# Performance work log

Hardware: AMD Instinct MI355X
Metric: run time of the kernel (lower is better)

The kernel has to match this reference:

```python
import jax, jax.numpy as jnp
import numpy as np

B, N, D, H, R = 4, 2048, 256, 8, 64
DH = D // H          # head dim = 32
K_SPARSE = 32        # top-k neighbors kept per query row
BN_EPS = 1e-5


def setup_inputs() -> dict:
    key = jax.random.key(0)
    ks = jax.random.split(key, 16)
    s_in = 1.0 / np.sqrt(D)
    s_r = 1.0 / np.sqrt(R)
    def lr(k1, k2):
        return (jax.random.normal(k1, (D, R), jnp.float32) * s_in,
                jax.random.normal(k2, (R, D), jnp.float32) * s_r)
    U_np, V_np = lr(ks[0], ks[1])
    U_q, V_q = lr(ks[2], ks[3])
    U_k, V_k = lr(ks[4], ks[5])
    U_v, V_v = lr(ks[6], ks[7])
    U_o, V_o = lr(ks[8], ks[9])
    U_op, V_op = lr(ks[10], ks[11])
    return {
        'x': jax.random.normal(ks[12], (B, N, D), jnp.float32),
        'U_np': U_np, 'V_np': V_np, 'b_np': jnp.zeros((D,), jnp.float32),
        'U_q': U_q, 'V_q': V_q,
        'U_k': U_k, 'V_k': V_k,
        'U_v': U_v, 'V_v': V_v,
        'U_o': U_o, 'V_o': V_o, 'b_o': jnp.zeros((D,), jnp.float32),
        'U_op': U_op, 'V_op': V_op, 'b_op': jnp.zeros((D,), jnp.float32),
        'gamma': jnp.ones((D,), jnp.float32),
        'beta': jnp.zeros((D,), jnp.float32),
    }


def _low_rank(x, U, V, b=None):
    y = (x @ U) @ V  # [..., D] -> [..., R] -> [..., D]
    return y + b if b is not None else y


def _heads(t):  # [B,N,D] -> [B,H,N,DH]
    return t.reshape(B, N, H, DH).transpose(0, 2, 1, 3)


def reference(x, U_np, V_np, b_np, U_q, V_q, U_k, V_k, U_v, V_v,
              U_o, V_o, b_o, U_op, V_op, b_op, gamma, beta):
    # node_proj: low-rank projection
    h = _low_rank(x, U_np, V_np, b_np)                      # [B,N,D]
    # low-rank sparse attention (q=k=v=h)
    q = _heads(_low_rank(h, U_q, V_q))                      # [B,H,N,DH]
    k = _heads(_low_rank(h, U_k, V_k))
    v = _heads(_low_rank(h, U_v, V_v))
    scores = jnp.einsum('bhnd,bhmd->bhnm', q, k) / jnp.sqrt(jnp.float32(DH))
    # topk sparsity: keep the K_SPARSE largest scores per query row
    thr = jax.lax.top_k(scores, K_SPARSE)[0][..., -1:]      # [B,H,N,1]
    neg_inf = jnp.finfo(scores.dtype).min
    scores = jnp.where(scores >= thr, scores, neg_inf)
    attn = jax.nn.softmax(scores, axis=-1)                  # [B,H,N,N]
    o = jnp.einsum('bhnm,bhmd->bhnd', attn, v)              # [B,H,N,DH]
    o = o.transpose(0, 2, 1, 3).reshape(B, N, D)
    o = _low_rank(o, U_o, V_o, b_o)                         # attention out proj
    # out_proj
    out = _low_rank(o, U_op, V_op, b_op)                    # [B,N,D]
    # BatchNorm1d over channel dim (stats over B and N, training-mode batch stats)
    mu = out.mean(axis=(0, 1))
    var = out.var(axis=(0, 1))
    out = (out - mu) * jax.lax.rsqrt(var + BN_EPS) * gamma + beta
    return out
```

## Files before the change

kernel.cpp:

```cpp
#include <hip/hip_runtime.h>
#include <hip/hip_bf16.h>

#define BB 4
#define NN 2048
#define DD 256
#define HH 8
#define RR 64
#define DHH 32
#define KSP 32
#define ROWS (BB*NN)
#define NEG_INF (-3.0e38f)

typedef __attribute__((ext_vector_type(8))) short bf16x8;
typedef __attribute__((ext_vector_type(4))) float f32x4;
#define MFMA16(A,B,C) __builtin_amdgcn_mfma_f32_16x16x32_bf16((A),(B),(C),0,0,0)

__global__ __launch_bounds__(64) void k_node_proj(
    const float* __restrict__ x, const float* __restrict__ U,
    const float* __restrict__ V, const float* __restrict__ bias,
    float* __restrict__ h)
{
    const int row = blockIdx.x, lane = threadIdx.x;
    __shared__ float xs[DD];
    __shared__ float ts[RR];
    const float* xr = x + (size_t)row * DD;
    { float4 t4 = ((const float4*)xr)[lane];
      xs[lane*4]=t4.x; xs[lane*4+1]=t4.y; xs[lane*4+2]=t4.z; xs[lane*4+3]=t4.w; }
    __syncthreads();
    float t = 0.f;
    for (int d = 0; d < DD; ++d) t = fmaf(xs[d], U[d*RR + lane], t);
    ts[lane] = t;
    __syncthreads();
    float a[4];
    #pragma unroll
    for (int j = 0; j < 4; ++j) a[j] = bias[lane + 64*j];
    for (int r = 0; r < RR; ++r) {
        float tv = ts[r];
        const float* Vr = V + r*DD + lane;
        #pragma unroll
        for (int j = 0; j < 4; ++j) a[j] = fmaf(tv, Vr[64*j], a[j]);
    }
    float* hr = h + (size_t)row * DD;
    #pragma unroll
    for (int j = 0; j < 4; ++j) hr[lane + 64*j] = a[j];
}

__global__ __launch_bounds__(64) void k_qkv(
    const float* __restrict__ h,
    const float* __restrict__ Uq, const float* __restrict__ Vq,
    const float* __restrict__ Uk, const float* __restrict__ Vk,
    const float* __restrict__ Uv, const float* __restrict__ Vv,
    float* __restrict__ q, float* __restrict__ k, float* __restrict__ v)
{
    const int row = blockIdx.x, lane = threadIdx.x;
    __shared__ float hs[DD];
    __shared__ float tq[RR], tk[RR], tvv[RR];
    const float* hr = h + (size_t)row * DD;
    { float4 t4 = ((const float4*)hr)[lane];
      hs[lane*4]=t4.x; hs[lane*4+1]=t4.y; hs[lane*4+2]=t4.z; hs[lane*4+3]=t4.w; }
    __syncthreads();
    float aq=0.f, ak=0.f, av=0.f;
    for (int d = 0; d < DD; ++d) {
        float hv = hs[d];
        aq = fmaf(hv, Uq[d*RR + lane], aq);
        ak = fmaf(hv, Uk[d*RR + lane], ak);
        av = fmaf(hv, Uv[d*RR + lane], av);
    }
    tq[lane]=aq; tk[lane]=ak; tvv[lane]=av;
    __syncthreads();
    float oq[4], ok[4], ov[4];
    #pragma unroll
    for (int j = 0; j < 4; ++j) { oq[j]=0.f; ok[j]=0.f; ov[j]=0.f; }
    for (int r = 0; r < RR; ++r) {
        float sq=tq[r], sk=tk[r], sv=tvv[r];
        const int base = r*DD + lane;
        #pragma unroll
        for (int j = 0; j < 4; ++j) {
            oq[j] = fmaf(sq, Vq[base + 64*j], oq[j]);
            ok[j] = fmaf(sk, Vk[base + 64*j], ok[j]);
            ov[j] = fmaf(sv, Vv[base + 64*j], ov[j]);
        }
    }
    float* qr = q + (size_t)row * DD;
    float* kr = k + (size_t)row * DD;
    float* vr = v + (size_t)row * DD;
    #pragma unroll
    for (int j = 0; j < 4; ++j) {
        qr[lane + 64*j] = oq[j];
        kr[lane + 64*j] = ok[j];
        vr[lane + 64*j] = ov[j];
    }
}

__device__ __forceinline__ unsigned short f2bf(float x) {
    __hip_bfloat16 h = __float2bfloat16(x);
    return *reinterpret_cast<unsigned short*>(&h);
}
__device__ __forceinline__ float bf2f(unsigned short u) {
    __hip_bfloat16 h; *reinterpret_cast<unsigned short*>(&h) = u;
    return __bfloat162float(h);
}
__device__ __forceinline__ void split3(float x, unsigned short& b1,
                                       unsigned short& b2, unsigned short& b3) {
    b1 = f2bf(x);        float f1 = bf2f(b1);
    float r = x - f1;    b2 = f2bf(r);
    float f2 = bf2f(b2); float r2 = r - f2;
    b3 = f2bf(r2);
}

#define CEX(a_, b_) { float _l = fminf(a_, b_); (b_) = fmaxf(a_, b_); (a_) = _l; }

__global__ __launch_bounds__(256)
__attribute__((amdgpu_waves_per_eu(3, 4)))
void k_attn(
    const float* __restrict__ qx, const float* __restrict__ kx,
    const float* __restrict__ vx, float* __restrict__ o)
{
    __shared__ float arena[4][2048];
    __shared__ float swl[256];
    __shared__ uint4 q3buf[256];
    const int tid  = threadIdx.x;
    const int lane = tid & 63;
    const int wv   = tid >> 6;
    const int blk  = blockIdx.x;
    const int tile = blk & 31;
    const int head = (blk >> 5) & 7;
    const int b    = blk >> 8;
    const float scale = 0.17677669529663687f;

    float* aw  = arena[wv];
    unsigned int* kbu = (unsigned int*)aw;
    float* scW = aw;
    float* vbW = aw + 1152;

    const float* Kb = kx + (size_t)b*NN*DD + head*DHH;
    const float* Vb = vx + (size_t)b*NN*DD + head*DHH;
    const int j0 = wv*512;

    bf16x8 aq[4][2];
    {
        const int qr = lane & 15, ko = (lane >> 4) * 8;
        const float* qbase = qx + ((size_t)(b*NN + tile*64))*DD + head*DHH + ko;
        #pragma unroll
        for (int t = 0; t < 4; ++t) {
            const float* qp = qbase + (size_t)(t*16 + qr)*DD;
            float4 x0 = ((const float4*)qp)[0];
            float4 x1 = ((const float4*)qp)[1];
            float xv[8] = {x0.x,x0.y,x0.z,x0.w,x1.x,x1.y,x1.z,x1.w};
            unsigned int w3[4];
            #pragma unroll
            for (int i = 0; i < 4; ++i) {
                unsigned short a1,a2,a3, b1,b2,b3;
                split3(xv[2*i]*scale,   a1, a2, a3);
                split3(xv[2*i+1]*scale, b1, b2, b3);
                aq[t][0][2*i]   = (short)a1;  aq[t][0][2*i+1] = (short)b1;
                aq[t][1][2*i]   = (short)a2;  aq[t][1][2*i+1] = (short)b2;
                w3[i] = (unsigned int)a3 | ((unsigned int)b3 << 16);
            }
            if (wv == 0) q3buf[t*64 + lane] = make_uint4(w3[0],w3[1],w3[2],w3[3]);
        }
    }
    __syncthreads();

    const int skey = lane >> 2, sgrp = lane & 3;
    const float* kSrc = Kb + (size_t)skey*DD + sgrp*8;
    const float* vSrc = Vb + (size_t)skey*DD + sgrp*8;

    auto convwrite_k = [&](float4 f0, float4 f1) {
        float xv[8] = {f0.x,f0.y,f0.z,f0.w,f1.x,f1.y,f1.z,f1.w};
        unsigned int w1[4], w2[4], w3[4];
        #pragma unroll
        for (int i = 0; i < 4; ++i) {
            unsigned short a0,b0,c0,a1,b1,c1;
            split3(xv[2*i],   a0, b0, c0);
            split3(xv[2*i+1], a1, b1, c1);
            w1[i] = (unsigned int)a0 | ((unsigned int)a1 << 16);
            w2[i] = (unsigned int)b0 | ((unsigned int)b1 << 16);
            w3[i] = (unsigned int)c0 | ((unsigned int)c1 << 16);
        }
        *(uint4*)(kbu + ( 0 + skey)*20 + sgrp*4) = make_uint4(w1[0],w1[1],w1[2],w1[3]);
        *(uint4*)(kbu + (16 + skey)*20 + sgrp*4) = make_uint4(w2[0],w2[1],w2[2],w2[3]);
        *(uint4*)(kbu + (32 + skey)*20 + sgrp*4) = make_uint4(w3[0],w3[1],w3[2],w3[3]);
    };

    auto scores_chunk = [&]() {
        const unsigned short* kb16 = (const unsigned short*)kbu;
        const int key = lane & 15, ko = (lane >> 4) * 8;
        bf16x8 bk0 = *(const bf16x8*)(kb16 + ( 0 + key)*40 + ko);
        bf16x8 bk1 = *(const bf16x8*)(kb16 + (16 + key)*40 + ko);
        bf16x8 bk2 = *(const bf16x8*)(kb16 + (32 + key)*40 + ko);
        const int qr0 = (lane >> 4) * 4;
        #pragma unroll
        for (int t = 0; t < 4; ++t) {
            uint4 qw = q3buf[t*64 + lane];
            bf16x8 q3 = *reinterpret_cast<const bf16x8*>(&qw);
            f32x4 c4 = {0.f, 0.f, 0.f, 0.f};
            c4 = MFMA16(aq[t][0], bk0, c4);
            c4 = MFMA16(aq[t][0], bk1, c4);
            c4 = MFMA16(aq[t][1], bk0, c4);
            c4 = MFMA16(aq[t][0], bk2, c4);
            c4 = MFMA16(q3,       bk0, c4);
            c4 = MFMA16(aq[t][1], bk1, c4);
            #pragma unroll
            for (int r = 0; r < 4; ++r)
                scW[(t*16 + qr0 + r)*18 + key] = c4[r];
        }
    };

    auto merge_batch = [&](float* t, float* sb) {
        #pragma unroll
        for (int i = 0; i < 8; ++i) CEX(sb[2*i], sb[2*i+1]);
        #pragma unroll
        for (int g = 0; g < 4; ++g) { CEX(sb[4*g], sb[4*g+2]); CEX(sb[4*g+1], sb[4*g+3]); }
        #pragma unroll
        for (int g = 0; g < 4; ++g) CEX(sb[4*g+1], sb[4*g+2]);
        #pragma unroll
        for (int g = 0; g < 2; ++g) {
            CEX(sb[8*g],   sb[8*g+4]); CEX(sb[8*g+1], sb[8*g+5]);
            CEX(sb[8*g+2], sb[8*g+6]); CEX(sb[8*g+3], sb[8*g+7]);
        }
        #pragma unroll
        for (int g = 0; g < 2; ++g) { CEX(sb[8*g+2], sb[8*g+4]); CEX(sb[8*g+3], sb[8*g+5]); }
        #pragma unroll
        for (int g = 0; g < 2; ++g) {
            CEX(sb[8*g+1], sb[8*g+2]); CEX(sb[8*g+3], sb[8*g+4]); CEX(sb[8*g+5], sb[8*g+6]);
        }
        #pragma unroll
        for (int i = 0; i < 8; ++i) CEX(sb[i], sb[i+8]);
        #pragma unroll
        for (int i = 0; i < 4; ++i) CEX(sb[i+4], sb[i+8]);
        #pragma unroll
        for (int g = 0; g < 3; ++g) { CEX(sb[4*g+2], sb[4*g+4]); CEX(sb[4*g+3], sb[4*g+5]); }
        #pragma unroll
        for (int i = 0; i < 7; ++i) CEX(sb[2*i+1], sb[2*i+2]);
        float u[16];
        #pragma unroll
        for (int i = 0; i < 16; ++i) u[i] = fmaxf(t[i], sb[15-i]);
        #pragma unroll
        for (int st = 8; st >= 1; st >>= 1)
            #pragma unroll
            for (int i = 0; i < 16; ++i)
                if ((i & st) == 0) CEX(u[i], u[i+st]);
        #pragma unroll
        for (int i = 0; i < 8; ++i) {
            float hi1 = t[31-i], hi2 = t[16+i];
            float u1 = u[i],     u2 = u[15-i];
            t[i]    = fminf(u1, hi1);
            t[31-i] = fmaxf(u1, hi1);
            t[15-i] = fminf(u2, hi2);
            t[16+i] = fmaxf(u2, hi2);
        }
        #pragma unroll
        for (int st = 8; st >= 1; st >>= 1)
            #pragma unroll
            for (int i = 0; i < 32; ++i)
                if ((i & st) == 0) CEX(t[i], t[i+st]);
    };

    float t32[32];
    #pragma unroll
    for (int i = 0; i < 32; ++i) t32[i] = NEG_INF;

    {
        float4 k0, k1;
        { const float* p = kSrc + (size_t)j0*DD;
          k0 = ((const float4*)p)[0]; k1 = ((const float4*)p)[1]; }
        convwrite_k(k0, k1);
        for (int c = 0; c < 32; ++c) {
            if (c + 1 < 32) {
                const float* p = kSrc + (size_t)(j0 + (c+1)*16)*DD;
                k0 = ((const float4*)p)[0]; k1 = ((const float4*)p)[1];
            }
            scores_chunk();
            {
                const float2* sp = (const float2*)(scW + lane*18);
                float sb[16];
                #pragma unroll
                for (int i = 0; i < 8; ++i) { float2 v2 = sp[i]; sb[2*i] = v2.x; sb[2*i+1] = v2.y; }
                merge_batch(t32, sb);
            }
            if (c + 1 < 32) convwrite_k(k0, k1);
        }
    }
    #pragma unroll
    for (int i = 0; i < 32; ++i) aw[i*64 + lane] = t32[i];
    __syncthreads();

    int i0=31, i1=31, i2=31, i3=31;
    float m = NEG_INF, thr = NEG_INF;
    for (int p = 0; p < 32; ++p) {
        float v0 = arena[0][i0*64 + lane];
        float v1 = arena[1][i1*64 + lane];
        float v2 = arena[2][i2*64 + lane];
        float v3 = arena[3][i3*64 + lane];
        float vm = fmaxf(fmaxf(v0,v1), fmaxf(v2,v3));
        if (p == 0) m = vm;
        thr = vm;
        if      (vm == v0) --i0;
        else if (vm == v1) --i1;
        else if (vm == v2) --i2;
        else               --i3;
    }
    __syncthreads();

    float acc[32];
    #pragma unroll
    for (int d = 0; d < 32; ++d) acc[d] = 0.f;
    float sw = 0.f;

    {
        float4 k0, k1, v0, v1;
        { const float* p = kSrc + (size_t)j0*DD;
          k0 = ((const float4*)p)[0]; k1 = ((const float4*)p)[1]; }
        { const float* p = vSrc + (size_t)j0*DD;
          v0 = ((const float4*)p)[0]; v1 = ((const float4*)p)[1]; }
        convwrite_k(k0, k1);
        { float* wp = vbW + skey*36 + sgrp*8;
          *(float4*)wp = v0; *(float4*)(wp + 4) = v1; }
        for (int c = 0; c < 32; ++c) {
            if (c + 1 < 32) {
                const float* p = kSrc + (size_t)(j0 + (c+1)*16)*DD;
                k0 = ((const float4*)p)[0]; k1 = ((const float4*)p)[1];
                const float* pv = vSrc + (size_t)(j0 + (c+1)*16)*DD;
                v0 = ((const float4*)pv)[0]; v1 = ((const float4*)pv)[1];
            }
            scores_chunk();
            const float2* sp = (const float2*)(scW + lane*18);
            #pragma unroll
            for (int i = 0; i < 8; ++i) {
                float2 s2 = sp[i];
                #pragma unroll
                for (int hs = 0; hs < 2; ++hs) {
                    float s = hs ? s2.y : s2.x;
                    int kk = 2*i + hs;
                    bool sel = (s >= thr);
                    float w = sel ? __expf(s - m) : 0.f;
                    sw += w;
                    if (__any(sel)) {
                        const float4* vv = (const float4*)(vbW + kk*36);
                        #pragma unroll
                        for (int r = 0; r < 8; ++r) {
                            float4 vvv = vv[r];
                            acc[4*r]   = fmaf(w, vvv.x, acc[4*r]);
                            acc[4*r+1] = fmaf(w, vvv.y, acc[4*r+1]);
                            acc[4*r+2] = fmaf(w, vvv.z, acc[4*r+2]);
                            acc[4*r+3] = fmaf(w, vvv.w, acc[4*r+3]);
                        }
                    }
                }
            }
            if (c + 1 < 32) {
                convwrite_k(k0, k1);
                float* wp = vbW + skey*36 + sgrp*8;
                *(float4*)wp = v0; *(float4*)(wp + 4) = v1;
            }
        }
    }

    #pragma unroll
    for (int d = 0; d < 32; ++d) aw[d*64 + lane] = acc[d];
    swl[wv*64 + lane] = sw;
    __syncthreads();

    float swsum = swl[lane] + swl[64+lane] + swl[128+lane] + swl[192+lane];
    float inv = 1.0f / swsum;
    float* orow = o + ((size_t)(b*NN + tile*64 + lane))*DD + head*DHH;
    #pragma unroll
    for (int dd = 0; dd < 8; ++dd) {
        int d = 8*wv + dd;
        float sv = arena[0][d*64+lane] + arena[1][d*64+lane]
                 + arena[2][d*64+lane] + arena[3][d*64+lane];
        orow[d] = sv * inv;
    }
}

__global__ __launch_bounds__(64) void k_out_proj(
    const float* __restrict__ o,
    const float* __restrict__ Uo,  const float* __restrict__ Vo,  const float* __restrict__ bo,
    const float* __restrict__ Uop, const float* __restrict__ Vop, const float* __restrict__ bop,
    float* __restrict__ outp)
{
    const int row = blockIdx.x, lane = threadIdx.x;
    __shared__ float buf[DD];
    __shared__ float ts[RR];
    const float* orow = o + (size_t)row * DD;
    { float4 t4 = ((const float4*)orow)[lane];
      buf[lane*4]=t4.x; buf[lane*4+1]=t4.y; buf[lane*4+2]=t4.z; buf[lane*4+3]=t4.w; }
    __syncthreads();
    float t = 0.f;
    for (int d = 0; d < DD; ++d) t = fmaf(buf[d], Uo[d*RR + lane], t);
    ts[lane] = t;
    __syncthreads();
    float a[4];
    #pragma unroll
    for (int j = 0; j < 4; ++j) a[j] = bo[lane + 64*j];
    for (int r = 0; r < RR; ++r) {
        float tv = ts[r];
        #pragma unroll
        for (int j = 0; j < 4; ++j) a[j] = fmaf(tv, Vo[r*DD + lane + 64*j], a[j]);
    }
    __syncthreads();
    #pragma unroll
    for (int j = 0; j < 4; ++j) buf[lane + 64*j] = a[j];
    __syncthreads();
    float t2 = 0.f;
    for (int d = 0; d < DD; ++d) t2 = fmaf(buf[d], Uop[d*RR + lane], t2);
    __syncthreads();
    ts[lane] = t2;
    __syncthreads();
    float c[4];
    #pragma unroll
    for (int j = 0; j < 4; ++j) c[j] = bop[lane + 64*j];
    for (int r = 0; r < RR; ++r) {
        float tv = ts[r];
        #pragma unroll
        for (int j = 0; j < 4; ++j) c[j] = fmaf(tv, Vop[r*DD + lane + 64*j], c[j]);
    }
    float* orow_out = outp + (size_t)row * DD;
    #pragma unroll
    for (int j = 0; j < 4; ++j) orow_out[lane + 64*j] = c[j];
}

__global__ __launch_bounds__(256) void k_bnpart(
    const float* __restrict__ outp, float* __restrict__ part)
{
    const int blk = blockIdx.x, t = threadIdx.x;
    const float* p = outp + (size_t)blk*64*DD + t;
    float s = 0.f, s2 = 0.f;
    #pragma unroll 4
    for (int r = 0; r < 64; ++r) {
        float v = p[(size_t)r*DD];
        s += v; s2 += v*v;
    }
    part[blk*512 + t]       = s;
    part[blk*512 + 256 + t] = s2;
}

__global__ __launch_bounds__(256) void k_bnfin(
    const float* __restrict__ part, float* __restrict__ stats,
    const float* __restrict__ gamma, const float* __restrict__ beta)
{
    const int c = threadIdx.x;
    float s = 0.f, s2 = 0.f;
    for (int j = 0; j < 128; ++j) {
        s  += part[j*512 + c];
        s2 += part[j*512 + 256 + c];
    }
    float mean = s * (1.0f/ROWS);
    float var  = s2 * (1.0f/ROWS) - mean*mean;
    float inv  = rsqrtf(var + 1e-5f);
    float g = gamma[c], be = beta[c];
    stats[c]      = g * inv;
    stats[DD + c] = be - mean * g * inv;
}

__global__ __launch_bounds__(256) void k_bnapply(
    const float* __restrict__ outp, const float* __restrict__ stats,
    float* __restrict__ out)
{
    const size_t idx = (size_t)blockIdx.x * 256 + threadIdx.x;
    const int c = (int)(idx & (DD-1));
    out[idx] = outp[idx] * stats[c] + stats[DD + c];
}

extern "C" void kernel_launch(void* const* d_in, const int* in_sizes, int n_in,
                              void* d_out, int out_size, void* d_ws, size_t ws_size,
                              hipStream_t stream)
{
    (void)in_sizes; (void)n_in; (void)out_size; (void)ws_size;
    const float* x    = (const float*)d_in[0];
    const float* U_np = (const float*)d_in[1];
    const float* V_np = (const float*)d_in[2];
    const float* b_np = (const float*)d_in[3];
    const float* U_q  = (const float*)d_in[4];
    const float* V_q  = (const float*)d_in[5];
    const float* U_k  = (const float*)d_in[6];
    const float* V_k  = (const float*)d_in[7];
    const float* U_v  = (const float*)d_in[8];
    const float* V_v  = (const float*)d_in[9];
    const float* U_o  = (const float*)d_in[10];
    const float* V_o  = (const float*)d_in[11];
    const float* b_o  = (const float*)d_in[12];
    const float* U_op = (const float*)d_in[13];
    const float* V_op = (const float*)d_in[14];
    const float* b_op = (const float*)d_in[15];
    const float* gamma= (const float*)d_in[16];
    const float* beta = (const float*)d_in[17];

    float* ws  = (float*)d_ws;
    float* out = (float*)d_out;
    const size_t BUF = (size_t)ROWS * DD;

    float* h    = out;
    float* q    = ws;
    float* k    = ws + BUF;
    float* v    = ws + 2*BUF;
    float* o    = out;
    float* outp = q;
    float* stats= k;
    float* part = v;

    k_node_proj<<<ROWS, 64, 0, stream>>>(x, U_np, V_np, b_np, h);
    k_qkv<<<ROWS, 64, 0, stream>>>(h, U_q, V_q, U_k, V_k, U_v, V_v, q, k, v);
    k_attn<<<BB*HH*32, 256, 0, stream>>>(q, k, v, o);
    k_out_proj<<<ROWS, 64, 0, stream>>>(o, U_o, V_o, b_o, U_op, V_op, b_op, outp);
    k_bnpart<<<128, 256, 0, stream>>>(outp, part);
    k_bnfin<<<1, 256, 0, stream>>>(part, stats, gamma, beta);
    k_bnapply<<<ROWS, 256, 0, stream>>>(outp, stats, out);
}
```

Measured before the change: 470.6 us.

## Process multiple rows per block in low-rank projections and pad score stride

The node, QKV and output projection kernels now handle 8 (or 4) rows per 64-thread block. Each weight element loaded from global memory is reused across several rows instead of being re-read once per row, which cuts the weight traffic that dominated these per-row kernels. In the attention kernel, the score scratch stride changes from 18 to an odd 19, with scalar reads replacing float2 reads, to avoid LDS bank conflicts; the V buffer offset is moved to fit the larger scratch. Fewer blocks launch and each thread holds more registers, which lowers parallelism and occupancy.

```diff
diff --git a/kernel.cpp b/kernel.cpp
--- a/kernel.cpp
+++ b/kernel.cpp
@@ -10,6 +10,7 @@
 #define KSP 32
 #define ROWS (BB*NN)
 #define NEG_INF (-3.0e38f)
+#define SSTR 19
 
 typedef __attribute__((ext_vector_type(8))) short bf16x8;
 typedef __attribute__((ext_vector_type(4))) float f32x4;
@@ -20,29 +21,50 @@
     const float* __restrict__ V, const float* __restrict__ bias,
     float* __restrict__ h)
 {
-    const int row = blockIdx.x, lane = threadIdx.x;
-    __shared__ float xs[DD];
-    __shared__ float ts[RR];
-    const float* xr = x + (size_t)row * DD;
-    { float4 t4 = ((const float4*)xr)[lane];
-      xs[lane*4]=t4.x; xs[lane*4+1]=t4.y; xs[lane*4+2]=t4.z; xs[lane*4+3]=t4.w; }
-    __syncthreads();
-    float t = 0.f;
-    for (int d = 0; d < DD; ++d) t = fmaf(xs[d], U[d*RR + lane], t);
-    ts[lane] = t;
-    __syncthreads();
-    float a[4];
-    #pragma unroll
-    for (int j = 0; j < 4; ++j) a[j] = bias[lane + 64*j];
-    for (int r = 0; r < RR; ++r) {
-        float tv = ts[r];
-        const float* Vr = V + r*DD + lane;
-        #pragma unroll
-        for (int j = 0; j < 4; ++j) a[j] = fmaf(tv, Vr[64*j], a[j]);
-    }
-    float* hr = h + (size_t)row * DD;
-    #pragma unroll
-    for (int j = 0; j < 4; ++j) hr[lane + 64*j] = a[j];
+    const int blk = blockIdx.x, lane = threadIdx.x;
+    const int row0 = blk * 8;
+    __shared__ float xs[8][DD];
+    __shared__ float ts[8][RR];
+    #pragma unroll
+    for (int r = 0; r < 8; ++r) {
+        float4 t4 = ((const float4*)(x + (size_t)(row0 + r)*DD))[lane];
+        *(float4*)&xs[r][lane*4] = t4;
+    }
+    __syncthreads();
+    float t[8];
+    #pragma unroll
+    for (int r = 0; r < 8; ++r) t[r] = 0.f;
+    for (int d = 0; d < DD; ++d) {
+        float u = U[d*RR + lane];
+        #pragma unroll
+        for (int r = 0; r < 8; ++r) t[r] = fmaf(xs[r][d], u, t[r]);
+    }
+    #pragma unroll
+    for (int r = 0; r < 8; ++r) ts[r][lane] = t[r];
+    __syncthreads();
+    float a[8][4];
+    #pragma unroll
+    for (int r = 0; r < 8; ++r)
+        #pragma unroll
+        for (int j = 0; j < 4; ++j) a[r][j] = bias[lane + 64*j];
+    for (int rr = 0; rr < RR; ++rr) {
+        float tv[8];
+        #pragma unroll
+        for (int r = 0; r < 8; ++r) tv[r] = ts[r][rr];
+        const float* Vr = V + rr*DD + lane;
+        #pragma unroll
+        for (int j = 0; j < 4; ++j) {
+            float vv = Vr[64*j];
+            #pragma unroll
+            for (int r = 0; r < 8; ++r) a[r][j] = fmaf(tv[r], vv, a[r][j]);
+        }
+    }
+    #pragma unroll
+    for (int r = 0; r < 8; ++r) {
+        float* hr = h + (size_t)(row0 + r)*DD;
+        #pragma unroll
+        for (int j = 0; j < 4; ++j) hr[lane + 64*j] = a[r][j];
+    }
 }
 
 __global__ __launch_bounds__(64) void k_qkv(
@@ -52,43 +74,68 @@
     const float* __restrict__ Uv, const float* __restrict__ Vv,
     float* __restrict__ q, float* __restrict__ k, float* __restrict__ v)
 {
-    const int row = blockIdx.x, lane = threadIdx.x;
-    __shared__ float hs[DD];
-    __shared__ float tq[RR], tk[RR], tvv[RR];
-    const float* hr = h + (size_t)row * DD;
-    { float4 t4 = ((const float4*)hr)[lane];
-      hs[lane*4]=t4.x; hs[lane*4+1]=t4.y; hs[lane*4+2]=t4.z; hs[lane*4+3]=t4.w; }
-    __syncthreads();
-    float aq=0.f, ak=0.f, av=0.f;
+    const int blk = blockIdx.x, lane = threadIdx.x;
+    const int row0 = blk * 4;
+    __shared__ float hs[4][DD];
+    __shared__ float tq[4][RR], tk[4][RR], tvv[4][RR];
+    #pragma unroll
+    for (int r = 0; r < 4; ++r) {
+        float4 t4 = ((const float4*)(h + (size_t)(row0 + r)*DD))[lane];
+        *(float4*)&hs[r][lane*4] = t4;
+    }
+    __syncthreads();
+    float aq[4], ak[4], av[4];
+    #pragma unroll
+    for (int r = 0; r < 4; ++r) { aq[r]=0.f; ak[r]=0.f; av[r]=0.f; }
     for (int d = 0; d < DD; ++d) {
-        float hv = hs[d];
-        aq = fmaf(hv, Uq[d*RR + lane], aq);
-        ak = fmaf(hv, Uk[d*RR + lane], ak);
-        av = fmaf(hv, Uv[d*RR + lane], av);
-    }
-    tq[lane]=aq; tk[lane]=ak; tvv[lane]=av;
-    __syncthreads();
-    float oq[4], ok[4], ov[4];
-    #pragma unroll
-    for (int j = 0; j < 4; ++j) { oq[j]=0.f; ok[j]=0.f; ov[j]=0.f; }
-    for (int r = 0; r < RR; ++r) {
-        float sq=tq[r], sk=tk[r], sv=tvv[r];
-        const int base = r*DD + lane;
+        float uq = Uq[d*RR + lane];
+        float uk = Uk[d*RR + lane];
+        float uv = Uv[d*RR + lane];
+        #pragma unroll
+        for (int r = 0; r < 4; ++r) {
+            float hv = hs[r][d];
+            aq[r] = fmaf(hv, uq, aq[r]);
+            ak[r] = fmaf(hv, uk, ak[r]);
+            av[r] = fmaf(hv, uv, av[r]);
+        }
+    }
+    #pragma unroll
+    for (int r = 0; r < 4; ++r) { tq[r][lane]=aq[r]; tk[r][lane]=ak[r]; tvv[r][lane]=av[r]; }
+    __syncthreads();
+    float oq[4][4], ok[4][4], ov[4][4];
+    #pragma unroll
+    for (int r = 0; r < 4; ++r)
+        #pragma unroll
+        for (int j = 0; j < 4; ++j) { oq[r][j]=0.f; ok[r][j]=0.f; ov[r][j]=0.f; }
+    for (int rr = 0; rr < RR; ++rr) {
+        float sq[4], sk[4], sv[4];
+        #pragma unroll
+        for (int r = 0; r < 4; ++r) { sq[r]=tq[r][rr]; sk[r]=tk[r][rr]; sv[r]=tvv[r][rr]; }
+        const int base = rr*DD + lane;
         #pragma unroll
         for (int j = 0; j < 4; ++j) {
-            oq[j] = fmaf(sq, Vq[base + 64*j], oq[j]);
-            ok[j] = fmaf(sk, Vk[base + 64*j], ok[j]);
-            ov[j] = fmaf(sv, Vv[base + 64*j], ov[j]);
-        }
-    }
-    float* qr = q + (size_t)row * DD;
-    float* kr = k + (size_t)row * DD;
-    float* vr = v + (size_t)row * DD;
-    #pragma unroll
-    for (int j = 0; j < 4; ++j) {
-        qr[lane + 64*j] = oq[j];
-        kr[lane + 64*j] = ok[j];
-        vr[lane + 64*j] = ov[j];
+            float wq = Vq[base + 64*j];
+            float wk = Vk[base + 64*j];
+            float wv = Vv[base + 64*j];
+            #pragma unroll
+            for (int r = 0; r < 4; ++r) {
+                oq[r][j] = fmaf(sq[r], wq, oq[r][j]);
+                ok[r][j] = fmaf(sk[r], wk, ok[r][j]);
+                ov[r][j] = fmaf(sv[r], wv, ov[r][j]);
+            }
+        }
+    }
+    #pragma unroll
+    for (int r = 0; r < 4; ++r) {
+        float* qr = q + (size_t)(row0 + r)*DD;
+        float* kr = k + (size_t)(row0 + r)*DD;
+        float* vr = v + (size_t)(row0 + r)*DD;
+        #pragma unroll
+        for (int j = 0; j < 4; ++j) {
+            qr[lane + 64*j] = oq[r][j];
+            kr[lane + 64*j] = ok[r][j];
+            vr[lane + 64*j] = ov[r][j];
+        }
     }
 }
 
@@ -131,7 +178,7 @@
     float* aw  = arena[wv];
     unsigned int* kbu = (unsigned int*)aw;
     float* scW = aw;
-    float* vbW = aw + 1152;
+    float* vbW = aw + 1216;
 
     const float* Kb = kx + (size_t)b*NN*DD + head*DHH;
     const float* Vb = vx + (size_t)b*NN*DD + head*DHH;
@@ -203,7 +250,7 @@
             c4 = MFMA16(aq[t][1], bk1, c4);
             #pragma unroll
             for (int r = 0; r < 4; ++r)
-                scW[(t*16 + qr0 + r)*18 + key] = c4[r];
+                scW[(t*16 + qr0 + r)*SSTR + key] = c4[r];
         }
     };
 
@@ -273,10 +320,10 @@
             }
             scores_chunk();
             {
-                const float2* sp = (const float2*)(scW + lane*18);
+                const float* sp = scW + lane*SSTR;
                 float sb[16];
                 #pragma unroll
-                for (int i = 0; i < 8; ++i) { float2 v2 = sp[i]; sb[2*i] = v2.x; sb[2*i+1] = v2.y; }
+                for (int i = 0; i < 16; ++i) sb[i] = sp[i];
                 merge_batch(t32, sb);
             }
             if (c + 1 < 32) convwrite_k(k0, k1);
@@ -325,27 +372,22 @@
                 v0 = ((const float4*)pv)[0]; v1 = ((const float4*)pv)[1];
             }
             scores_chunk();
-            const float2* sp = (const float2*)(scW + lane*18);
-            #pragma unroll
-            for (int i = 0; i < 8; ++i) {
-                float2 s2 = sp[i];
-                #pragma unroll
-                for (int hs = 0; hs < 2; ++hs) {
-                    float s = hs ? s2.y : s2.x;
-                    int kk = 2*i + hs;
-                    bool sel = (s >= thr);
-                    float w = sel ? __expf(s - m) : 0.f;
-                    sw += w;
-                    if (__any(sel)) {
-                        const float4* vv = (const float4*)(vbW + kk*36);
-                        #pragma unroll
-                        for (int r = 0; r < 8; ++r) {
-                            float4 vvv = vv[r];
-                            acc[4*r]   = fmaf(w, vvv.x, acc[4*r]);
-                            acc[4*r+1] = fmaf(w, vvv.y, acc[4*r+1]);
-                            acc[4*r+2] = fmaf(w, vvv.z, acc[4*r+2]);
-                            acc[4*r+3] = fmaf(w, vvv.w, acc[4*r+3]);
-                        }
+            const float* sp = scW + lane*SSTR;
+            #pragma unroll
+            for (int kk = 0; kk < 16; ++kk) {
+                float s = sp[kk];
+                bool sel = (s >= thr);
+                float w = sel ? __expf(s - m) : 0.f;
+                sw += w;
+                if (__any(sel)) {
+                    const float4* vv = (const float4*)(vbW + kk*36);
+                    #pragma unroll
+                    for (int r = 0; r < 8; ++r) {
+                        float4 vvv = vv[r];
+                        acc[4*r]   = fmaf(w, vvv.x, acc[4*r]);
+                        acc[4*r+1] = fmaf(w, vvv.y, acc[4*r+1]);
+                        acc[4*r+2] = fmaf(w, vvv.z, acc[4*r+2]);
+                        acc[4*r+3] = fmaf(w, vvv.w, acc[4*r+3]);
                     }
                 }
             }
@@ -380,45 +422,85 @@
     const float* __restrict__ Uop, const float* __restrict__ Vop, const float* __restrict__ bop,
     float* __restrict__ outp)
 {
-    const int row = blockIdx.x, lane = threadIdx.x;
-    __shared__ float buf[DD];
-    __shared__ float ts[RR];
-    const float* orow = o + (size_t)row * DD;
-    { float4 t4 = ((const float4*)orow)[lane];
-      buf[lane*4]=t4.x; buf[lane*4+1]=t4.y; buf[lane*4+2]=t4.z; buf[lane*4+3]=t4.w; }
-    __syncthreads();
-    float t = 0.f;
-    for (int d = 0; d < DD; ++d) t = fmaf(buf[d], Uo[d*RR + lane], t);
-    ts[lane] = t;
-    __syncthreads();
-    float a[4];
-    #pragma unroll
-    for (int j = 0; j < 4; ++j) a[j] = bo[lane + 64*j];
-    for (int r = 0; r < RR; ++r) {
-        float tv = ts[r];
-        #pragma unroll
-        for (int j = 0; j < 4; ++j) a[j] = fmaf(tv, Vo[r*DD + lane + 64*j], a[j]);
-    }
-    __syncthreads();
-    #pragma unroll
-    for (int j = 0; j < 4; ++j) buf[lane + 64*j] = a[j];
-    __syncthreads();
-    float t2 = 0.f;
-    for (int d = 0; d < DD; ++d) t2 = fmaf(buf[d], Uop[d*RR + lane], t2);
-    __syncthreads();
-    ts[lane] = t2;
-    __syncthreads();
-    float c[4];
-    #pragma unroll
-    for (int j = 0; j < 4; ++j) c[j] = bop[lane + 64*j];
-    for (int r = 0; r < RR; ++r) {
-        float tv = ts[r];
-        #pragma unroll
-        for (int j = 0; j < 4; ++j) c[j] = fmaf(tv, Vop[r*DD + lane + 64*j], c[j]);
-    }
-    float* orow_out = outp + (size_t)row * DD;
-    #pragma unroll
-    for (int j = 0; j < 4; ++j) orow_out[lane + 64*j] = c[j];
+    const int blk = blockIdx.x, lane = threadIdx.x;
+    const int row0 = blk * 8;
+    __shared__ float buf[8][DD];
+    __shared__ float ts[8][RR];
+    #pragma unroll
+    for (int r = 0; r < 8; ++r) {
+        float4 t4 = ((const float4*)(o + (size_t)(row0 + r)*DD))[lane];
+        *(float4*)&buf[r][lane*4] = t4;
+    }
+    __syncthreads();
+    float t[8];
+    #pragma unroll
+    for (int r = 0; r < 8; ++r) t[r] = 0.f;
+    for (int d = 0; d < DD; ++d) {
+        float u = Uo[d*RR + lane];
+        #pragma unroll
+        for (int r = 0; r < 8; ++r) t[r] = fmaf(buf[r][d], u, t[r]);
+    }
+    #pragma unroll
+    for (int r = 0; r < 8; ++r) ts[r][lane] = t[r];
+    __syncthreads();
+    float a[8][4];
+    #pragma unroll
+    for (int r = 0; r < 8; ++r)
+        #pragma unroll
+        for (int j = 0; j < 4; ++j) a[r][j] = bo[lane + 64*j];
+    for (int rr = 0; rr < RR; ++rr) {
+        float tv[8];
+        #pragma unroll
+        for (int r = 0; r < 8; ++r) tv[r] = ts[r][rr];
+        const float* Vr = Vo + rr*DD + lane;
+        #pragma unroll
+        for (int j = 0; j < 4; ++j) {
+            float vv = Vr[64*j];
+            #pragma unroll
+            for (int r = 0; r < 8; ++r) a[r][j] = fmaf(tv[r], vv, a[r][j]);
+        }
+    }
+    __syncthreads();
+    #pragma unroll
+    for (int r = 0; r < 8; ++r)
+        #pragma unroll
+        for (int j = 0; j < 4; ++j) buf[r][lane + 64*j] = a[r][j];
+    __syncthreads();
+    float t2[8];
+    #pragma unroll
+    for (int r = 0; r < 8; ++r) t2[r] = 0.f;
+    for (int d = 0; d < DD; ++d) {
+        float u = Uop[d*RR + lane];
+        #pragma unroll
+        for (int r = 0; r < 8; ++r) t2[r] = fmaf(buf[r][d], u, t2[r]);
+    }
+    __syncthreads();
+    #pragma unroll
+    for (int r = 0; r < 8; ++r) ts[r][lane] = t2[r];
+    __syncthreads();
+    float c2[8][4];
+    #pragma unroll
+    for (int r = 0; r < 8; ++r)
+        #pragma unroll
+        for (int j = 0; j < 4; ++j) c2[r][j] = bop[lane + 64*j];
+    for (int rr = 0; rr < RR; ++rr) {
+        float tv[8];
+        #pragma unroll
+        for (int r = 0; r < 8; ++r) tv[r] = ts[r][rr];
+        const float* Vr = Vop + rr*DD + lane;
+        #pragma unroll
+        for (int j = 0; j < 4; ++j) {
+            float vv = Vr[64*j];
+            #pragma unroll
+            for (int r = 0; r < 8; ++r) c2[r][j] = fmaf(tv[r], vv, c2[r][j]);
+        }
+    }
+    #pragma unroll
+    for (int r = 0; r < 8; ++r) {
+        float* orow_out = outp + (size_t)(row0 + r)*DD;
+        #pragma unroll
+        for (int j = 0; j < 4; ++j) orow_out[lane + 64*j] = c2[r][j];
+    }
 }
 
 __global__ __launch_bounds__(256) void k_bnpart(
@@ -500,10 +582,10 @@
     float* stats= k;
     float* part = v;
 
-    k_node_proj<<<ROWS, 64, 0, stream>>>(x, U_np, V_np, b_np, h);
-    k_qkv<<<ROWS, 64, 0, stream>>>(h, U_q, V_q, U_k, V_k, U_v, V_v, q, k, v);
+    k_node_proj<<<ROWS/8, 64, 0, stream>>>(x, U_np, V_np, b_np, h);
+    k_qkv<<<ROWS/4, 64, 0, stream>>>(h, U_q, V_q, U_k, V_k, U_v, V_v, q, k, v);
     k_attn<<<BB*HH*32, 256, 0, stream>>>(q, k, v, o);
-    k_out_proj<<<ROWS, 64, 0, stream>>>(o, U_o, V_o, b_o, U_op, V_op, b_op, outp);
+    k_out_proj<<<ROWS/8, 64, 0, stream>>>(o, U_o, V_o, b_o, U_op, V_op, b_op, outp);
     k_bnpart<<<128, 256, 0, stream>>>(outp, part);
     k_bnfin<<<1, 256, 0, stream>>>(part, stats, gamma, beta);
     k_bnapply<<<ROWS, 256, 0, stream>>>(outp, stats, out);
```

Result: faster. 434.9 us (-7.6%).
